# Optimization experiments

Measured on AMD Instinct MI355X. Metric: run time of the kernel, lower is better.

The kernel has to match this reference:

```python
import jax, jax.numpy as jnp
import numpy as np

N, E, K, F_IN, H = 50000, 640000, 3, 128, 128


def setup_inputs() -> dict:
    key = jax.random.key(0)
    ks = jax.random.split(key, 14)
    s = 0.05
    return {
        "x": jax.random.normal(ks[0], (N, F_IN), jnp.float32),
        "edge_index": jax.random.randint(ks[1], (2, E), 0, N, dtype=jnp.int32),
        "edge_weight": jax.random.uniform(ks[2], (E,), jnp.float32, minval=0.1, maxval=1.0),
        "W_x": jax.random.normal(ks[3], (4, F_IN, H), jnp.float32) * s,   # dense input weights (i,f,c,o)
        "w_c": jax.random.normal(ks[4], (3, H), jnp.float32) * s,         # peephole weights (i,f,o)
        "b": jax.random.normal(ks[5], (4, H), jnp.float32) * s,           # gate biases (i,f,c,o)
        "theta": jax.random.normal(ks[6], (4, K, H, H), jnp.float32) * s, # ChebConv weights per gate
        "theta_b": jax.random.normal(ks[7], (4, H), jnp.float32) * s,     # ChebConv biases per gate
        "gcn_w": jax.random.normal(ks[8], (H, H), jnp.float32) * s,
        "gcn_b": jnp.zeros((H,), jnp.float32),
        "bn_gamma": jnp.ones((H,), jnp.float32),
        "bn_beta": jnp.zeros((H,), jnp.float32),
        "bn_mean": jax.random.normal(ks[9], (H,), jnp.float32) * 0.1,
        "bn_var": jax.random.uniform(ks[10], (H,), jnp.float32, minval=0.5, maxval=1.5),
        "lin_w": jax.random.normal(ks[11], (H, 1), jnp.float32) * s,
        "lin_b": jnp.zeros((1,), jnp.float32),
    }


def reference(x, edge_index, edge_weight, W_x, w_c, b, theta, theta_b, gcn_w, gcn_b, bn_gamma, bn_beta, bn_mean, bn_var, lin_w, lin_b):
    n = x.shape[0]
    src, dst = edge_index[0], edge_index[1]

    # --- ChebConv normalization (sym, lambda_max=2): L_hat = -D^{-1/2} A D^{-1/2}, zero diagonal ---
    deg = jnp.zeros((n,), x.dtype).at[src].add(edge_weight)
    safe = jnp.where(deg > 0, deg, 1.0)
    dis = jnp.where(deg > 0, jax.lax.rsqrt(safe), 0.0)
    lw = -dis[src] * edge_weight * dis[dst]  # per-edge scaled-Laplacian weight

    def prop(h):  # out[i] = sum_{edges j->i} lw * h[j]
        return jnp.zeros_like(h).at[dst].add(lw[:, None] * h[src])

    def cheb(h, th, tb):  # sum_k T_k(L_hat) h @ theta_k + bias, Chebyshev recurrence
        Tx0, out = h, h @ th[0]
        Tx1 = prop(h)
        out = out + Tx1 @ th[1]
        for k in range(2, K):
            Tx2 = 2.0 * prop(Tx1) - Tx0
            out = out + Tx2 @ th[k]
            Tx0, Tx1 = Tx1, Tx2
        return out + tb

    # --- GCLSTM with H = C = 0 (module passes no initial state) ---
    Hs = jnp.zeros((n, W_x.shape[2]), x.dtype)
    Cs = jnp.zeros_like(Hs)
    I = jax.nn.sigmoid(x @ W_x[0] + cheb(Hs, theta[0], theta_b[0]) + w_c[0] * Cs + b[0])
    Fg = jax.nn.sigmoid(x @ W_x[1] + cheb(Hs, theta[1], theta_b[1]) + w_c[1] * Cs + b[1])
    T = jnp.tanh(x @ W_x[2] + cheb(Hs, theta[2], theta_b[2]) + b[2])
    Cs = Fg * Cs + I * T
    O = jax.nn.sigmoid(x @ W_x[3] + cheb(Hs, theta[3], theta_b[3]) + w_c[2] * Cs + b[3])
    Hs = O * jnp.tanh(Cs)

    # --- GCNConv(H) with unit edge weights + added self-loops ---
    h = Hs @ gcn_w
    deg_g = jnp.ones((n,), x.dtype).at[dst].add(jnp.ones((edge_index.shape[1],), x.dtype))
    dg = jax.lax.rsqrt(deg_g)
    g = jnp.zeros_like(h).at[dst].add((dg[src] * dg[dst])[:, None] * h[src]) + (dg * dg)[:, None] * h + gcn_b

    g = jax.nn.relu(g)
    g = bn_gamma * (g - bn_mean) * jax.lax.rsqrt(bn_var + 1e-5) + bn_beta  # BatchNorm1d (eval)
    return g @ lin_w + lin_b  # Dropout = identity in eval
```

## Files before the change

kernel.cpp:

```cpp
#include <hip/hip_runtime.h>
#include <hip/hip_bf16.h>

#define NN 50000
#define NE 640000
#define NP 196
#define CAP 64

typedef unsigned short ushort_t;
typedef unsigned int uint_t;
typedef __attribute__((ext_vector_type(8))) short bf16x8;
typedef __attribute__((ext_vector_type(4))) float f32x4;

__device__ __forceinline__ float b2f(ushort_t u) {
    union { uint_t u; float f; } v; v.u = ((uint_t)u) << 16; return v.f;
}
__device__ __forceinline__ ushort_t f2b(float f) {
    union { float f; uint_t u; } v; v.f = f;
    uint_t u = v.u;
    uint_t r = u + 0x7fffu + ((u >> 16) & 1u);
    return (ushort_t)(r >> 16);
}
__device__ __forceinline__ float fsig(float x)  { return __builtin_amdgcn_rcpf(1.0f + __expf(-x)); }
__device__ __forceinline__ float ftanh(float x) { return 1.0f - 2.0f * __builtin_amdgcn_rcpf(1.0f + __expf(2.0f * x)); }
__device__ __forceinline__ float ldm(const void* p, int i, int mf) {
    return mf ? ((const float*)p)[i] : b2f(((const ushort_t*)p)[i]);
}

#define OFF_HB   0
#define OFF_BSRC 12800000
#define OFF_CNT  25600000
#define OFF_WT   25800000
#define OFF_COEF 25931072
#define OFF_MODE 25933640
#define WS_REQ   25933648

__global__ void fb_k(ushort_t* __restrict__ out, int n) {
    int i = blockIdx.x * blockDim.x + threadIdx.x;
    if (i < n) out[i] = 0;
}

__global__ void init_k(const ushort_t* __restrict__ x, int* __restrict__ cnt,
                       int* __restrict__ mode) {
    __shared__ int s[256];
    int b = blockIdx.x, t = threadIdx.x;
    if (b < NP) {
        int i = b * 256 + t;
        if (i < NN) cnt[i] = 0;
    } else {
        int bad = 0;
        for (int i = t; i < 4096; i += 256) {
            int e = (x[i] >> 7) & 0xFF;
            if (e >= 0xC0) bad++;
        }
        s[t] = bad; __syncthreads();
        for (int o = 128; o >= 1; o >>= 1) { if (t < o) s[t] += s[t + o]; __syncthreads(); }
        if (t == 0) mode[0] = (s[0] > 8) ? 1 : 0;
    }
}

__global__ void prep_k(const void* __restrict__ Wx, const void* __restrict__ gcnw,
                       const void* __restrict__ wc, const void* __restrict__ bb,
                       const void* __restrict__ thb,
                       const void* __restrict__ gam, const void* __restrict__ bet,
                       const void* __restrict__ mea, const void* __restrict__ var,
                       const void* __restrict__ linw, const void* __restrict__ linb,
                       const int* __restrict__ mode,
                       ushort_t* __restrict__ WT, float* __restrict__ coef) {
    __shared__ float red[128];
    int b = blockIdx.x, t = threadIdx.x;
    int mf = mode[0];
    if (b < 64) {
        int gid = b * 256 + t;
        int f = gid >> 7, k = gid & 127;
        const int srcoff[4] = { 0, 2 * 16384, 3 * 16384, 0 };
        #pragma unroll
        for (int m = 0; m < 4; m++) {
            const void* S = (m == 3) ? gcnw : Wx;
            WT[m * 16384 + gid] = f2b(ldm(S, srcoff[m] + k * 128 + f, mf));
        }
    } else {
        if (t < 128) {
            float rs = rsqrtf(ldm(var, t, mf) + 1e-5f);
            float ga = ldm(gam, t, mf);
            float lw = ldm(linw, t, mf);
            coef[t]       = ldm(thb, t, mf)           + ldm(bb, t, mf);
            coef[128 + t] = ldm(thb, 2 * 128 + t, mf) + ldm(bb, 2 * 128 + t, mf);
            coef[256 + t] = ldm(thb, 3 * 128 + t, mf) + ldm(bb, 3 * 128 + t, mf);
            coef[384 + t] = ldm(wc, 2 * 128 + t, mf);
            coef[512 + t] = ga * rs * lw;
            red[t] = (ldm(bet, t, mf) - ldm(mea, t, mf) * ga * rs) * lw;
        }
        __syncthreads();
        for (int off = 64; off >= 1; off >>= 1) {
            if (t < off && t < 128) red[t] += red[t + off];
            __syncthreads();
        }
        if (t == 0) coef[640] = red[0] + ldm(linb, 0, mf);
    }
}

__global__ void fill_k(const int* __restrict__ ei, int* __restrict__ cnt,
                       int* __restrict__ bsrc) {
    int tid = blockIdx.x * blockDim.x + threadIdx.x;
    if (tid >= NE / 4) return;
    int4 s4 = ((const int4*)ei)[tid];
    int4 d4 = ((const int4*)(ei + NE))[tid];
    int p0 = atomicAdd(&cnt[d4.x], 1);
    int p1 = atomicAdd(&cnt[d4.y], 1);
    int p2 = atomicAdd(&cnt[d4.z], 1);
    int p3 = atomicAdd(&cnt[d4.w], 1);
    if (p0 < CAP) bsrc[d4.x * CAP + p0] = s4.x;
    if (p1 < CAP) bsrc[d4.y * CAP + p1] = s4.y;
    if (p2 < CAP) bsrc[d4.z * CAP + p2] = s4.z;
    if (p3 < CAP) bsrc[d4.w * CAP + p3] = s4.w;
}

__launch_bounds__(256)
__global__ void gates_k(const void* __restrict__ x, const ushort_t* __restrict__ WT,
                        const float* __restrict__ coef, const int* __restrict__ cnt,
                        const int* __restrict__ mode, ushort_t* __restrict__ hb) {
    __shared__ ushort_t tile[64 * 136];
    __shared__ float ldsdg[64];
    int t = threadIdx.x;
    int base = blockIdx.x * 64;
    int mf = mode[0];

    if (t < 64) {
        int n = base + t;
        int c = (n < NN) ? cnt[n] : 0;
        if (c < 0) c = 0;
        ldsdg[t] = rsqrtf(1.0f + (float)c);
    }
    for (int i = 0; i < 4; i++) {
        int idx = (i * 256 + t) * 8;
        int row = idx >> 7, col = idx & 127;
        int n = base + row;
        bf16x8 v;
        if (n >= NN) {
            v = (bf16x8)0;
        } else if (mf == 0) {
            v = *(const bf16x8*)((const ushort_t*)x + n * 128 + col);
        } else {
            const float* xf = (const float*)x + n * 128 + col;
            float4 lo = *(const float4*)xf;
            float4 hi = *(const float4*)(xf + 4);
            v[0] = (short)f2b(lo.x); v[1] = (short)f2b(lo.y);
            v[2] = (short)f2b(lo.z); v[3] = (short)f2b(lo.w);
            v[4] = (short)f2b(hi.x); v[5] = (short)f2b(hi.y);
            v[6] = (short)f2b(hi.z); v[7] = (short)f2b(hi.w);
        }
        *(bf16x8*)&tile[row * 136 + col] = v;
    }
    __syncthreads();

    int lane = t & 63, wave = t >> 6;
    int m = lane & 15, quad = lane >> 4;

    bf16x8 a[4][4];
    #pragma unroll
    for (int rt = 0; rt < 4; rt++)
        #pragma unroll
        for (int kt = 0; kt < 4; kt++)
            a[rt][kt] = *(const bf16x8*)&tile[(rt * 16 + m) * 136 + kt * 32 + quad * 8];
    __syncthreads();

    const ushort_t* WTi = WT;
    const ushort_t* WTc = WT + 16384;
    const ushort_t* WTo = WT + 2 * 16384;

    #pragma unroll
    for (int ft = 0; ft < 2; ft++) {
        int f = wave * 32 + ft * 16 + m;
        bf16x8 bi[4], bc[4], bo[4];
        #pragma unroll
        for (int kt = 0; kt < 4; kt++) {
            int off = f * 128 + kt * 32 + quad * 8;
            bi[kt] = *(const bf16x8*)(WTi + off);
            bc[kt] = *(const bf16x8*)(WTc + off);
            bo[kt] = *(const bf16x8*)(WTo + off);
        }
        float bi_f = coef[f], bc_f = coef[128 + f], bo_f = coef[256 + f], w2 = coef[384 + f];
        #pragma unroll
        for (int rt = 0; rt < 4; rt++) {
            f32x4 ai = {0,0,0,0}, ac = {0,0,0,0}, ao = {0,0,0,0};
            #pragma unroll
            for (int kt = 0; kt < 4; kt++) {
                ai = __builtin_amdgcn_mfma_f32_16x16x32_bf16(a[rt][kt], bi[kt], ai, 0, 0, 0);
                ac = __builtin_amdgcn_mfma_f32_16x16x32_bf16(a[rt][kt], bc[kt], ac, 0, 0, 0);
                ao = __builtin_amdgcn_mfma_f32_16x16x32_bf16(a[rt][kt], bo[kt], ao, 0, 0, 0);
            }
            #pragma unroll
            for (int r = 0; r < 4; r++) {
                float I  = fsig(ai[r] + bi_f);
                float T  = ftanh(ac[r] + bc_f);
                float Cs = I * T;
                float O  = fsig(ao[r] + w2 * Cs + bo_f);
                float Hs = O * ftanh(Cs);
                tile[(rt * 16 + quad * 4 + r) * 136 + f] = f2b(Hs);
            }
        }
    }
    __syncthreads();

    const ushort_t* WTg = WT + 3 * 16384;
    bf16x8 ah[4][4];
    #pragma unroll
    for (int rt = 0; rt < 4; rt++)
        #pragma unroll
        for (int kt = 0; kt < 4; kt++)
            ah[rt][kt] = *(const bf16x8*)&tile[(rt * 16 + m) * 136 + kt * 32 + quad * 8];

    #pragma unroll
    for (int ft = 0; ft < 2; ft++) {
        int f = wave * 32 + ft * 16 + m;
        bf16x8 bg[4];
        #pragma unroll
        for (int kt = 0; kt < 4; kt++)
            bg[kt] = *(const bf16x8*)(WTg + f * 128 + kt * 32 + quad * 8);
        #pragma unroll
        for (int rt = 0; rt < 4; rt++) {
            f32x4 acc = {0,0,0,0};
            #pragma unroll
            for (int kt = 0; kt < 4; kt++)
                acc = __builtin_amdgcn_mfma_f32_16x16x32_bf16(ah[rt][kt], bg[kt], acc, 0, 0, 0);
            #pragma unroll
            for (int r = 0; r < 4; r++) {
                int n = base + rt * 16 + quad * 4 + r;
                if (n < NN)
                    hb[n * 128 + f] = f2b(ldsdg[rt * 16 + quad * 4 + r] * acc[r]);
            }
        }
    }
}

__launch_bounds__(256)
__global__ void gat_out_k(const ushort_t* __restrict__ hb, const int* __restrict__ cnt,
                          const int* __restrict__ bsrc,
                          const void* __restrict__ gcnb, const float* __restrict__ coef,
                          const int* __restrict__ mode, void* __restrict__ out) {
    int wid  = (blockIdx.x * blockDim.x + threadIdx.x) >> 6;
    int lane = threadIdx.x & 63;
    if (wid >= NN) return;
    int half = lane >> 5, sl = lane & 31;
    int c = cnt[wid]; if (c < 0) c = 0;
    int deg = (c < CAP) ? c : CAP;
    const int* brow = bsrc + wid * CAP;

    float a0 = 0.0f, a1 = 0.0f, a2 = 0.0f, a3 = 0.0f;
    int j = half;
    for (; j + 2 < deg; j += 4) {
        int s0 = brow[j], s1 = brow[j + 2];
        uint2 r0 = *(const uint2*)(hb + s0 * 128 + sl * 4);
        uint2 r1 = *(const uint2*)(hb + s1 * 128 + sl * 4);
        a0 += b2f((ushort_t)(r0.x & 0xffffu)) + b2f((ushort_t)(r1.x & 0xffffu));
        a1 += b2f((ushort_t)(r0.x >> 16))     + b2f((ushort_t)(r1.x >> 16));
        a2 += b2f((ushort_t)(r0.y & 0xffffu)) + b2f((ushort_t)(r1.y & 0xffffu));
        a3 += b2f((ushort_t)(r0.y >> 16))     + b2f((ushort_t)(r1.y >> 16));
    }
    if (j < deg) {
        int s = brow[j];
        uint2 r = *(const uint2*)(hb + s * 128 + sl * 4);
        a0 += b2f((ushort_t)(r.x & 0xffffu));
        a1 += b2f((ushort_t)(r.x >> 16));
        a2 += b2f((ushort_t)(r.y & 0xffffu));
        a3 += b2f((ushort_t)(r.y >> 16));
    }
    if (half == 0) {
        uint2 r = *(const uint2*)(hb + wid * 128 + sl * 4);
        a0 += b2f((ushort_t)(r.x & 0xffffu));
        a1 += b2f((ushort_t)(r.x >> 16));
        a2 += b2f((ushort_t)(r.y & 0xffffu));
        a3 += b2f((ushort_t)(r.y >> 16));
    }
    a0 += __shfl_xor(a0, 32); a1 += __shfl_xor(a1, 32);
    a2 += __shfl_xor(a2, 32); a3 += __shfl_xor(a3, 32);
    int mf = mode[0];
    float d = rsqrtf(1.0f + (float)c);
    int fb = sl * 4;
    float g0 = d * a0 + ldm(gcnb, fb,     mf);
    float g1 = d * a1 + ldm(gcnb, fb + 1, mf);
    float g2 = d * a2 + ldm(gcnb, fb + 2, mf);
    float g3 = d * a3 + ldm(gcnb, fb + 3, mf);
    float v = fmaxf(g0, 0.0f) * coef[512 + fb]
            + fmaxf(g1, 0.0f) * coef[512 + fb + 1]
            + fmaxf(g2, 0.0f) * coef[512 + fb + 2]
            + fmaxf(g3, 0.0f) * coef[512 + fb + 3];
    #pragma unroll
    for (int o = 32; o >= 1; o >>= 1) v += __shfl_down(v, o);
    if (lane == 0) {
        float r = 0.5f * v + coef[640];
        if (mf) ((float*)out)[wid] = r;
        else    ((ushort_t*)out)[wid] = f2b(r);
    }
}

extern "C" void kernel_launch(void* const* d_in, const int* in_sizes, int n_in,
                              void* d_out, int out_size, void* d_ws, size_t ws_size,
                              hipStream_t stream) {
    if (ws_size < (size_t)WS_REQ) {
        fb_k<<<(out_size + 255) / 256, 256, 0, stream>>>((ushort_t*)d_out, out_size);
        return;
    }
    const void* x    = d_in[0];
    const int*  ei   = (const int*)d_in[1];
    const void* Wx   = d_in[3];
    const void* wc   = d_in[4];
    const void* bb   = d_in[5];
    const void* thb  = d_in[7];
    const void* gcnw = d_in[8];
    const void* gcnb = d_in[9];
    const void* gam  = d_in[10];
    const void* bet  = d_in[11];
    const void* mea  = d_in[12];
    const void* var  = d_in[13];
    const void* linw = d_in[14];
    const void* linb = d_in[15];

    char* ws = (char*)d_ws;
    ushort_t* hb   = (ushort_t*)(ws + OFF_HB);
    int*      bsrc = (int*)     (ws + OFF_BSRC);
    int*      cnt  = (int*)     (ws + OFF_CNT);
    ushort_t* WT   = (ushort_t*)(ws + OFF_WT);
    float*    coef = (float*)   (ws + OFF_COEF);
    int*      mode = (int*)     (ws + OFF_MODE);

    init_k<<<NP + 1, 256, 0, stream>>>((const ushort_t*)x, cnt, mode);
    prep_k<<<65, 256, 0, stream>>>(Wx, gcnw, wc, bb, thb, gam, bet, mea, var, linw, linb, mode, WT, coef);
    fill_k<<<(NE / 4 + 255) / 256, 256, 0, stream>>>(ei, cnt, bsrc);
    gates_k<<<(NN + 63) / 64, 256, 0, stream>>>(x, WT, coef, cnt, mode, hb);
    gat_out_k<<<(NN * 64 + 255) / 256, 256, 0, stream>>>(hb, cnt, bsrc, gcnb, coef, mode, d_out);
}
```

Baseline: 201.1 us.

## Fuse edge-bucketing into gates kernel and move source-degree scaling to gather

The separate fill kernel and the gates kernel become one launch. Blocks are interleaved 5 gate blocks to 4 fill blocks, so the atomic bucketing of edges overlaps with the MFMA gate computation. Because gates no longer waits for the degree counts, the per-source normalization dg[src] is now applied in the gather kernel. That kernel reads cnt[src] per edge, and the next source indices are prefetched with a masked index. The weight-transpose prep is also vectorized to 8 elements per thread, which halves its block count. The trade-off is an extra random cnt load and rsqrt per edge in the gather.

```diff
diff --git a/kernel.cpp b/kernel.cpp
--- a/kernel.cpp
+++ b/kernel.cpp
@@ -5,6 +5,8 @@
 #define NE 640000
 #define NP 196
 #define CAP 64
+#define NGB 782
+#define NFB 625
 
 typedef unsigned short ushort_t;
 typedef unsigned int uint_t;
@@ -69,15 +71,28 @@
     __shared__ float red[128];
     int b = blockIdx.x, t = threadIdx.x;
     int mf = mode[0];
-    if (b < 64) {
+    if (b < 32) {
         int gid = b * 256 + t;
-        int f = gid >> 7, k = gid & 127;
+        int m  = gid >> 11;
+        int u  = gid & 2047;
+        int k  = u >> 4;
+        int f0 = (u & 15) << 3;
         const int srcoff[4] = { 0, 2 * 16384, 3 * 16384, 0 };
-        #pragma unroll
-        for (int m = 0; m < 4; m++) {
-            const void* S = (m == 3) ? gcnw : Wx;
-            WT[m * 16384 + gid] = f2b(ldm(S, srcoff[m] + k * 128 + f, mf));
-        }
+        const void* S = (m == 3) ? gcnw : Wx;
+        int sbase = srcoff[m] + k * 128 + f0;
+        ushort_t vals[8];
+        if (mf == 0) {
+            bf16x8 v = *(const bf16x8*)((const ushort_t*)S + sbase);
+            #pragma unroll
+            for (int i = 0; i < 8; i++) vals[i] = (ushort_t)v[i];
+        } else {
+            const float* Sf = (const float*)S + sbase;
+            #pragma unroll
+            for (int i = 0; i < 8; i++) vals[i] = f2b(Sf[i]);
+        }
+        ushort_t* D = WT + m * 16384 + k;
+        #pragma unroll
+        for (int i = 0; i < 8; i++) D[(f0 + i) * 128] = vals[i];
     } else {
         if (t < 128) {
             float rs = rsqrtf(ldm(var, t, mf) + 1e-5f);
@@ -99,38 +114,38 @@
     }
 }
 
-__global__ void fill_k(const int* __restrict__ ei, int* __restrict__ cnt,
+__launch_bounds__(256)
+__global__ void gafi_k(const void* __restrict__ x, const ushort_t* __restrict__ WT,
+                       const float* __restrict__ coef, const int* __restrict__ mode,
+                       ushort_t* __restrict__ hb,
+                       const int* __restrict__ ei, int* __restrict__ cnt,
                        int* __restrict__ bsrc) {
-    int tid = blockIdx.x * blockDim.x + threadIdx.x;
-    if (tid >= NE / 4) return;
-    int4 s4 = ((const int4*)ei)[tid];
-    int4 d4 = ((const int4*)(ei + NE))[tid];
-    int p0 = atomicAdd(&cnt[d4.x], 1);
-    int p1 = atomicAdd(&cnt[d4.y], 1);
-    int p2 = atomicAdd(&cnt[d4.z], 1);
-    int p3 = atomicAdd(&cnt[d4.w], 1);
-    if (p0 < CAP) bsrc[d4.x * CAP + p0] = s4.x;
-    if (p1 < CAP) bsrc[d4.y * CAP + p1] = s4.y;
-    if (p2 < CAP) bsrc[d4.z * CAP + p2] = s4.z;
-    if (p3 < CAP) bsrc[d4.w * CAP + p3] = s4.w;
-}
-
-__launch_bounds__(256)
-__global__ void gates_k(const void* __restrict__ x, const ushort_t* __restrict__ WT,
-                        const float* __restrict__ coef, const int* __restrict__ cnt,
-                        const int* __restrict__ mode, ushort_t* __restrict__ hb) {
     __shared__ ushort_t tile[64 * 136];
-    __shared__ float ldsdg[64];
+    int per = blockIdx.x / 9, rem = blockIdx.x % 9;
     int t = threadIdx.x;
-    int base = blockIdx.x * 64;
+
+    if (rem >= 5) {
+        int fb = per * 4 + (rem - 5);
+        if (fb >= NFB) return;
+        int tid = fb * 256 + t;
+        int4 s4 = ((const int4*)ei)[tid];
+        int4 d4 = ((const int4*)(ei + NE))[tid];
+        int p0 = atomicAdd(&cnt[d4.x], 1);
+        int p1 = atomicAdd(&cnt[d4.y], 1);
+        int p2 = atomicAdd(&cnt[d4.z], 1);
+        int p3 = atomicAdd(&cnt[d4.w], 1);
+        if (p0 < CAP) bsrc[d4.x * CAP + p0] = s4.x;
+        if (p1 < CAP) bsrc[d4.y * CAP + p1] = s4.y;
+        if (p2 < CAP) bsrc[d4.z * CAP + p2] = s4.z;
+        if (p3 < CAP) bsrc[d4.w * CAP + p3] = s4.w;
+        return;
+    }
+
+    int gb = per * 5 + rem;
+    if (gb >= NGB) return;
+    int base = gb * 64;
     int mf = mode[0];
 
-    if (t < 64) {
-        int n = base + t;
-        int c = (n < NN) ? cnt[n] : 0;
-        if (c < 0) c = 0;
-        ldsdg[t] = rsqrtf(1.0f + (float)c);
-    }
     for (int i = 0; i < 4; i++) {
         int idx = (i * 256 + t) * 8;
         int row = idx >> 7, col = idx & 127;
@@ -226,8 +241,7 @@
             #pragma unroll
             for (int r = 0; r < 4; r++) {
                 int n = base + rt * 16 + quad * 4 + r;
-                if (n < NN)
-                    hb[n * 128 + f] = f2b(ldsdg[rt * 16 + quad * 4 + r] * acc[r]);
+                if (n < NN) hb[n * 128 + f] = f2b(acc[r]);
             }
         }
     }
@@ -247,35 +261,42 @@
     const int* brow = bsrc + wid * CAP;
 
     float a0 = 0.0f, a1 = 0.0f, a2 = 0.0f, a3 = 0.0f;
-    int j = half;
-    for (; j + 2 < deg; j += 4) {
-        int s0 = brow[j], s1 = brow[j + 2];
-        uint2 r0 = *(const uint2*)(hb + s0 * 128 + sl * 4);
-        uint2 r1 = *(const uint2*)(hb + s1 * 128 + sl * 4);
-        a0 += b2f((ushort_t)(r0.x & 0xffffu)) + b2f((ushort_t)(r1.x & 0xffffu));
-        a1 += b2f((ushort_t)(r0.x >> 16))     + b2f((ushort_t)(r1.x >> 16));
-        a2 += b2f((ushort_t)(r0.y & 0xffffu)) + b2f((ushort_t)(r1.y & 0xffffu));
-        a3 += b2f((ushort_t)(r0.y >> 16))     + b2f((ushort_t)(r1.y >> 16));
-    }
-    if (j < deg) {
-        int s = brow[j];
-        uint2 r = *(const uint2*)(hb + s * 128 + sl * 4);
-        a0 += b2f((ushort_t)(r.x & 0xffffu));
-        a1 += b2f((ushort_t)(r.x >> 16));
-        a2 += b2f((ushort_t)(r.y & 0xffffu));
-        a3 += b2f((ushort_t)(r.y >> 16));
-    }
+    int s0 = brow[half];
+    int s1 = brow[half + 2];
+    for (int j = half; j < deg; j += 4) {
+        int sn0 = brow[(j + 4) & (CAP - 1)];
+        int sn1 = brow[(j + 6) & (CAP - 1)];
+        {
+            int cs = cnt[s0]; if (cs < 0) cs = 0;
+            uint2 r = *(const uint2*)(hb + s0 * 128 + sl * 4);
+            float w = rsqrtf(1.0f + (float)cs);
+            a0 += w * b2f((ushort_t)(r.x & 0xffffu));
+            a1 += w * b2f((ushort_t)(r.x >> 16));
+            a2 += w * b2f((ushort_t)(r.y & 0xffffu));
+            a3 += w * b2f((ushort_t)(r.y >> 16));
+        }
+        if (j + 2 < deg) {
+            int cs = cnt[s1]; if (cs < 0) cs = 0;
+            uint2 r = *(const uint2*)(hb + s1 * 128 + sl * 4);
+            float w = rsqrtf(1.0f + (float)cs);
+            a0 += w * b2f((ushort_t)(r.x & 0xffffu));
+            a1 += w * b2f((ushort_t)(r.x >> 16));
+            a2 += w * b2f((ushort_t)(r.y & 0xffffu));
+            a3 += w * b2f((ushort_t)(r.y >> 16));
+        }
+        s0 = sn0; s1 = sn1;
+    }
+    float d = rsqrtf(1.0f + (float)c);
     if (half == 0) {
         uint2 r = *(const uint2*)(hb + wid * 128 + sl * 4);
-        a0 += b2f((ushort_t)(r.x & 0xffffu));
-        a1 += b2f((ushort_t)(r.x >> 16));
-        a2 += b2f((ushort_t)(r.y & 0xffffu));
-        a3 += b2f((ushort_t)(r.y >> 16));
+        a0 += d * b2f((ushort_t)(r.x & 0xffffu));
+        a1 += d * b2f((ushort_t)(r.x >> 16));
+        a2 += d * b2f((ushort_t)(r.y & 0xffffu));
+        a3 += d * b2f((ushort_t)(r.y >> 16));
     }
     a0 += __shfl_xor(a0, 32); a1 += __shfl_xor(a1, 32);
     a2 += __shfl_xor(a2, 32); a3 += __shfl_xor(a3, 32);
     int mf = mode[0];
-    float d = rsqrtf(1.0f + (float)c);
     int fb = sl * 4;
     float g0 = d * a0 + ldm(gcnb, fb,     mf);
     float g1 = d * a1 + ldm(gcnb, fb + 1, mf);
@@ -325,8 +346,7 @@
     int*      mode = (int*)     (ws + OFF_MODE);
 
     init_k<<<NP + 1, 256, 0, stream>>>((const ushort_t*)x, cnt, mode);
-    prep_k<<<65, 256, 0, stream>>>(Wx, gcnw, wc, bb, thb, gam, bet, mea, var, linw, linb, mode, WT, coef);
-    fill_k<<<(NE / 4 + 255) / 256, 256, 0, stream>>>(ei, cnt, bsrc);
-    gates_k<<<(NN + 63) / 64, 256, 0, stream>>>(x, WT, coef, cnt, mode, hb);
+    prep_k<<<33, 256, 0, stream>>>(Wx, gcnw, wc, bb, thb, gam, bet, mea, var, linw, linb, mode, WT, coef);
+    gafi_k<<<157 * 9, 256, 0, stream>>>(x, WT, coef, mode, hb, ei, cnt, bsrc);
     gat_out_k<<<(NN * 64 + 255) / 256, 256, 0, stream>>>(hb, cnt, bsrc, gcnb, coef, mode, d_out);
 }
```

After: 190.3 us. -5.4%, faster.
